# Optimization experiments

Hardware: AMD Instinct MI355X
Metric: run time of the kernel (lower is better)

## Reference

```python
import jax, jax.numpy as jnp
import numpy as np

B, T, Y, X, E, TR, R = 64, 1024, 512, 128, 512, 512, 512


def setup_inputs() -> dict:
    key = jax.random.key(0)
    ks = iter(jax.random.split(key, 48))

    def w(shape, s=0.05):
        return (jax.random.normal(next(ks), shape, jnp.float32) * s)

    z = lambda *s: jnp.zeros(s, jnp.float32)
    inp = dict(
        data=jax.random.uniform(next(ks), (B, T, Y), jnp.float32),
        eps_q=jax.random.normal(next(ks), (T, B, X), jnp.float32),
        eps_p=jax.random.normal(next(ks), (T, B, X), jnp.float32),
        # RNN (single layer, relu nonlinearity)
        rnn_Wih=w((Y, R)), rnn_Whh=w((R, R)), rnn_bih=z(R), rnn_bhh=z(R),
        h0=z(R), xq0=z(X), x0=z(X),
        # GaussianCombiner
        comb_Wxh=w((X, R)), comb_bxh=z(R),
        comb_Whm=w((R, X)), comb_bhm=z(X),
        comb_Whl=w((R, X)), comb_bhl=z(X),
        # GaussianGatedTransition
        t_Wg1=w((X, TR)), t_bg1=z(TR), t_Wg2=w((TR, X)), t_bg2=z(X),
        t_Wp1=w((X, TR)), t_bp1=z(TR), t_Wp2=w((TR, X)), t_bp2=z(X),
        t_Wmu=jnp.eye(X, dtype=jnp.float32), t_bmu=z(X),  # torch inits lin_x_to_mu to identity
        t_Wlv=w((X, X)), t_blv=z(X),
        # BernoulliEmitter
        e_W1=w((X, E)), e_b1=z(E), e_W2=w((E, E)), e_b2=z(E),
        e_W3=w((E, Y)), e_b3=z(Y),
    )
    return inp


def reference(data, eps_q, eps_p,
              rnn_Wih, rnn_Whh, rnn_bih, rnn_bhh, h0, xq0, x0,
              comb_Wxh, comb_bxh, comb_Whm, comb_bhm, comb_Whl, comb_bhl,
              t_Wg1, t_bg1, t_Wg2, t_bg2, t_Wp1, t_bp1, t_Wp2, t_bp2,
              t_Wmu, t_bmu, t_Wlv, t_blv,
              e_W1, e_b1, e_W2, e_b2, e_W3, e_b3):
    Bx = data.shape[0]

    # ---- inference RNN: run on time-reversed data, then reverse output back ----
    # precompute input projection for all steps: [T, B, R]
    x_proj = (jnp.einsum('bty,yr->btr', data[:, ::-1, :], rnn_Wih)
              + rnn_bih + rnn_bhh).transpose(1, 0, 2)

    def rnn_step(h, xp):
        h = jax.nn.relu(xp + h @ rnn_Whh)
        return h, h

    h_init = jnp.broadcast_to(h0, (Bx, R))
    _, hs = jax.lax.scan(rnn_step, h_init, x_proj)  # [T, B, R]
    rnn_out = hs[::-1]  # back to original time order, aligned with data

    # ---- inference network: sequential combiner + reparameterize ----
    def inf_step(x_prev, inputs):
        h_rnn, eps = inputs
        h_c = 0.5 * (jnp.tanh(x_prev @ comb_Wxh + comb_bxh) + h_rnn)
        mu = h_c @ comb_Whm + comb_bhm
        lv = h_c @ comb_Whl + comb_bhl
        x_t = mu + eps * jnp.exp(0.5 * lv)
        return x_t, (x_t, mu, lv)

    xq0b = jnp.broadcast_to(xq0, (Bx, X))
    _, (q_x, q_mu, q_lv) = jax.lax.scan(inf_step, xq0b, (rnn_out, eps_q))
    q_x, q_mu, q_lv = (a.transpose(1, 0, 2) for a in (q_x, q_mu, q_lv))  # [B,T,X]

    # ---- generative model: sequential gated transition ----
    def gen_step(x_prev, eps):
        gate = jax.nn.sigmoid(jax.nn.relu(x_prev @ t_Wg1 + t_bg1) @ t_Wg2 + t_bg2)
        pm = jax.nn.relu(x_prev @ t_Wp1 + t_bp1) @ t_Wp2 + t_bp2
        mu = (1.0 - gate) * (x_prev @ t_Wmu + t_bmu) + gate * pm
        lv = jax.nn.relu(pm) @ t_Wlv + t_blv
        x_t = mu + eps * jnp.exp(0.5 * lv)
        return x_t, (x_t, mu, lv)

    x0b = jnp.broadcast_to(x0, (Bx, X))
    _, (p_x, p_mu, p_lv) = jax.lax.scan(gen_step, x0b, eps_p)
    p_x, p_mu, p_lv = (a.transpose(1, 0, 2) for a in (p_x, p_mu, p_lv))  # [B,T,X]

    # ---- emitter over all (b, t) at once ----
    h1 = jax.nn.relu(jnp.einsum('btx,xe->bte', q_x, e_W1) + e_b1)
    h2 = jax.nn.relu(jnp.einsum('bte,ef->btf', h1, e_W2) + e_b2)
    y_probs = jax.nn.sigmoid(jnp.einsum('bte,ey->bty', h2, e_W3) + e_b3)

    return (q_x, q_mu, q_lv, p_x, p_mu, p_lv, y_probs)
```

## Files before the change

kernel.cpp:

```cpp
#include <hip/hip_runtime.h>
#include <stdint.h>

typedef __bf16 bf16x8 __attribute__((ext_vector_type(8)));
typedef short  s16x8  __attribute__((ext_vector_type(8)));
typedef float  f32x4  __attribute__((ext_vector_type(4)));

#define MFMA16(a, b, c) __builtin_amdgcn_mfma_f32_16x16x32_bf16((a), (b), (c), 0, 0, 0)

#define OFF_X      0ull
#define OFF_QXBF   67108864ull
#define OFF_WIH    83886080ull
#define OFF_WHH    84410368ull
#define OFF_WXH    84934656ull
#define OFF_WICAT  85065728ull
#define OFF_W1CAT  85327872ull
#define OFF_WG2    85590016ull
#define OFF_WP2    85721088ull
#define OFF_WMU    85852160ull
#define OFF_WLV    85884928ull
#define OFF_EW1    85917696ull
#define OFF_EW2    86048768ull
#define OFF_EW3    86573056ull
#define OFF_B1CAT  87097344ull
#define OFF_BICAT  87101440ull
#define OFF_HX     87102464ull
#define OFF_XPCNT  87364608ull
#define OFF_RNNF   87368704ull

#define QX_O  0ull
#define QMU_O 8388608ull
#define QLV_O 16777216ull
#define PX_O  25165824ull
#define PMU_O 33554432ull
#define PLV_O 41943040ull
#define Y_O   50331648ull

#define SMEM_SCAN 159744
#define SMEM_EMIS 133120

struct P {
  char* ws; float* out;
  const float *data, *eps_q, *eps_p;
  const float *Wih, *Whh, *bih, *bhh, *h0, *xq0, *x0;
  const float *Wxh, *bxh, *Whm, *bhm, *Whl, *bhl;
  const float *Wg1, *bg1, *Wg2, *bg2, *Wp1, *bp1, *Wp2, *bp2, *Wmu, *bmu, *Wlv, *blv;
  const float *eW1, *eb1, *eW2, *eb2, *eW3, *eb3;
};

__device__ __forceinline__ short f2bf(float f) {
  union { float f; uint32_t u; } v; v.f = f;
  uint32_t r = (v.u + 0x7FFFu + ((v.u >> 16) & 1u)) >> 16;
  return (short)(uint16_t)r;
}
__device__ __forceinline__ float bf2f(short s) {
  union { uint32_t u; float f; } v; v.u = ((uint32_t)(uint16_t)s) << 16;
  return v.f;
}
__device__ __forceinline__ bf16x8 ldfrag(const short* pp) { return *(const bf16x8*)pp; }
__device__ __forceinline__ bf16x8 cvt8p(const float* pp) {
  bf16x8 r;
#pragma unroll
  for (int i = 0; i < 8; ++i) r[i] = (__bf16)pp[i];
  return r;
}
__device__ __forceinline__ bf16x8 relu8(bf16x8 a) {
  s16x8 s = __builtin_bit_cast(s16x8, a);
#pragma unroll
  for (int i = 0; i < 8; ++i) s[i] = (s[i] < 0) ? (short)0 : s[i];
  return __builtin_bit_cast(bf16x8, s);
}

__device__ __forceinline__ void relfence() {
  asm volatile("s_waitcnt vmcnt(0)" ::: "memory");
}
__device__ __forceinline__ void st_sc16(short* pp, short v) {
  __hip_atomic_store(pp, v, __ATOMIC_RELAXED, __HIP_MEMORY_SCOPE_AGENT);
}
__device__ __forceinline__ short ld_sc16(const short* pp) {
  return __hip_atomic_load((short*)pp, __ATOMIC_RELAXED, __HIP_MEMORY_SCOPE_AGENT);
}
__device__ __forceinline__ unsigned long long ld_sc64(const void* pp) {
  return __hip_atomic_load((unsigned long long*)pp, __ATOMIC_RELAXED, __HIP_MEMORY_SCOPE_AGENT);
}
__device__ __forceinline__ bf16x8 ldfrag_sc(const short* pp) {
  union { unsigned long long q[2]; bf16x8 v; } u;
  u.q[0] = ld_sc64(pp);
  u.q[1] = ld_sc64(pp + 4);
  return u.v;
}
__device__ __forceinline__ int ldflag(int* pp) {
  return __hip_atomic_load(pp, __ATOMIC_RELAXED, __HIP_MEMORY_SCOPE_AGENT);
}
__device__ __forceinline__ void stflag(int* pp, int v) {
  __hip_atomic_store(pp, v, __ATOMIC_RELAXED, __HIP_MEMORY_SCOPE_AGENT);
}
__device__ __forceinline__ void waitf(int* f, int n, int target) {
  if (threadIdx.x < 64) {
    const int ln = threadIdx.x;
    while (1) {
      int v = (ln < n) ? ldflag(f + ln) : target;
      if (__all(v >= target)) break;
      __builtin_amdgcn_s_sleep(1);
    }
  }
  __syncthreads();
}
__device__ __forceinline__ void pubf(int* f, int val) {
  relfence();
  __syncthreads();
  if (threadIdx.x == 0) stflag(f, val);
}
__device__ __forceinline__ void cpy16(void* dst, const void* src, int n16) {
  float4* d = (float4*)dst; const float4* s = (const float4*)src;
  for (int i = threadIdx.x; i < n16; i += 256) d[i] = s[i];
}

__device__ __forceinline__ void pack_w(short* dst, const float* src, int KT, int N, int idx) {
  int tile = idx >> 9, rem = idx & 511;
  int lane = rem >> 3, j = rem & 7;
  int nt = tile / KT, kt = tile - nt * KT;
  int k = kt * 32 + ((lane >> 4) << 3) + j, n = (nt << 4) + (lane & 15);
  dst[idx] = f2bf(src[(int64_t)k * N + n]);
}

__global__ void __launch_bounds__(256) k_prep(P p) {
  char* ws = p.ws;
  const int64_t total = 1608032;
  for (int64_t i = (int64_t)blockIdx.x * 256 + threadIdx.x; i < total;
       i += (int64_t)gridDim.x * 256) {
    int64_t r = i;
    if (r < 262144) { pack_w((short*)(ws + OFF_WIH), p.Wih, 16, 512, (int)r); continue; }
    r -= 262144;
    if (r < 262144) { pack_w((short*)(ws + OFF_WHH), p.Whh, 16, 512, (int)r); continue; }
    r -= 262144;
    if (r < 65536) { pack_w((short*)(ws + OFF_WXH), p.Wxh, 4, 512, (int)r); continue; }
    r -= 65536;
    if (r < 131072) {
      int idx = (int)r;
      int tile = idx >> 9, rem = idx & 511, lane = rem >> 3, jj = rem & 7;
      int nt = tile >> 4, kt = tile & 15;
      int k = kt * 32 + ((lane >> 4) << 3) + jj, ccol = (nt << 4) + (lane & 15);
      int pair = ccol >> 7, within = ccol & 127, sub = within >> 6;
      int col = (within & 63) + (pair << 6);
      const float* s = sub ? p.Whl : p.Whm;
      ((short*)(ws + OFF_WICAT))[idx] = f2bf(s[(int64_t)k * 128 + col]);
      continue;
    }
// ... 5 lines not shown
      int k = kt * 32 + ((lane >> 4) << 3) + jj, ccol = (nt << 4) + (lane & 15);
      const float* s = (ccol < 512) ? p.Wg1 : p.Wp1;
      ((short*)(ws + OFF_W1CAT))[idx] = f2bf(s[(int64_t)k * 512 + (ccol & 511)]);
      continue;
    }
    r -= 131072;
    if (r < 65536) { pack_w((short*)(ws + OFF_WG2), p.Wg2, 16, 128, (int)r); continue; }
    r -= 65536;
    if (r < 65536) { pack_w((short*)(ws + OFF_WP2), p.Wp2, 16, 128, (int)r); continue; }
    r -= 65536;
    if (r < 16384) { pack_w((short*)(ws + OFF_WMU), p.Wmu, 4, 128, (int)r); continue; }
    r -= 16384;
    if (r < 16384) { pack_w((short*)(ws + OFF_WLV), p.Wlv, 4, 128, (int)r); continue; }
    r -= 16384;
    if (r < 65536) { pack_w((short*)(ws + OFF_EW1), p.eW1, 4, 512, (int)r); continue; }
    r -= 65536;
    if (r < 262144) { pack_w((short*)(ws + OFF_EW2), p.eW2, 16, 512, (int)r); continue; }
    r -= 262144;
    if (r < 262144) { pack_w((short*)(ws + OFF_EW3), p.eW3, 16, 512, (int)r); continue; }
    r -= 262144;
    if (r < 1024) { ((float*)(ws + OFF_B1CAT))[r] = (r < 512) ? p.bg1[r] : p.bp1[r - 512]; continue; }
    r -= 1024;
    if (r < 256) {
      int ccol = (int)r; int pair = ccol >> 7, within = ccol & 127, sub = within >> 6;
      int col = (within & 63) + (pair << 6);
      ((float*)(ws + OFF_BICAT))[ccol] = sub ? p.bhl[col] : p.bhm[col];
      continue;
    }
    r -= 256;
    ((int*)(ws + OFF_XPCNT))[r] = 0;
  }
}

__global__ void __launch_bounds__(256, 1) k_scan(P p) {
  extern __shared__ char smem[];
  char* ws = p.ws;
  const int tid = threadIdx.x;
  const int lane = tid & 63, w = tid >> 6;
  const int l16 = lane & 15, quad = lane >> 4;
  const int wg = blockIdx.x;

  short* Xb   = (short*)(ws + OFF_X);
  short* qxbf = (short*)(ws + OFF_QXBF);
  int* xp_cnt = (int*)(ws + OFF_XPCNT);

  if (wg < 64) {
    const int s = wg & 7, t0 = wg >> 3;
    const short* wih = (const short*)(ws + OFF_WIH);
    for (int tt = 0; tt < 128; ++tt) {
      const int t = t0 + (tt << 3);
      const int tsrc = 1023 - t;
      const float* arow = p.data + ((size_t)(w * 16 + l16) * 1024 + tsrc) * 512 + quad * 8;
      f32x4 acc[4] = {};
      for (int kt = 0; kt < 16; ++kt) {
        bf16x8 af = cvt8p(arow + kt * 32);
#pragma unroll
        for (int i = 0; i < 4; ++i) {
          const int nt = s * 4 + i;
          bf16x8 bw = ldfrag(wih + ((size_t)(nt * 16 + kt) * 64 + lane) * 8);
          acc[i] = MFMA16(af, bw, acc[i]);
        }
      }
      short* xrow = Xb + (size_t)t * 32768;
#pragma unroll
      for (int i = 0; i < 4; ++i) {
        const int col = (s * 4 + i) * 16 + l16;
        const float bias = p.bih[col] + p.bhh[col];
#pragma unroll
        for (int r = 0; r < 4; ++r) {
          const int row = w * 16 + quad * 4 + r;
          st_sc16(xrow + (size_t)row * 512 + col, f2bf(acc[i][r] + bias));
        }
      }
      relfence();
      __syncthreads();
      if (tid == 0) atomicAdd(xp_cnt + t, 1);
    }
    return;
  }

  if (wg < 72) {
    const int id = wg - 64, g = id >> 1, k = id & 1;
    int* rf = (int*)(ws + OFF_RNNF) + g * 4;
    short* hxb = (short*)(ws + OFF_HX);
    short* hl = (short*)smem;
    {
      const short* whh = (const short*)(ws + OFF_WHH);
      bf16x8 wb[4][16];
#pragma unroll
      for (int i = 0; i < 4; ++i) {
        const int nt = k * 16 + w * 4 + i;
#pragma unroll
        for (int kt = 0; kt < 16; ++kt)
          wb[i][kt] = ldfrag(whh + ((size_t)(nt * 16 + kt) * 64 + lane) * 8);
      }
      for (int t = 0; t < 1024; ++t) {
        if (tid < 64) {
          while (1) {
            int ok = 1;
            if (tid == 0) { if (t > 0) ok = (ldflag(rf + (1 - k)) >= t); }
            else if (tid == 1) ok = (ldflag(xp_cnt + t) >= 8);
            if (__all(ok)) break;
            __builtin_amdgcn_s_sleep(1);
          }
        }
        __syncthreads();
        bf16x8 af[16];
        short xv[4][4];
        if (t == 0) {
#pragma unroll
          for (int kt = 0; kt < 16; ++kt) af[kt] = cvt8p(p.h0 + kt * 32 + quad * 8);
        } else {
          const short* hs = hxb + (((size_t)(g * 2 + ((t - 1) & 1)) * 2 + (1 - k)) * 4096);
#pragma unroll
          for (int kt = 0; kt < 8; ++kt)
            af[(1 - k) * 8 + kt] = ldfrag_sc(hs + l16 * 256 + kt * 32 + quad * 8);
        }
        {
          const short* xrow = Xb + (size_t)t * 32768;
#pragma unroll
          for (int i = 0; i < 4; ++i) {
            const int col = k * 256 + (w * 4 + i) * 16 + l16;
#pragma unroll
            for (int r = 0; r < 4; ++r)
              xv[i][r] = ld_sc16(xrow + (size_t)(g * 16 + quad * 4 + r) * 512 + col);
          }
        }
        if (t > 0) {
#pragma unroll
          for (int kt = 0; kt < 8; ++kt)
            af[k * 8 + kt] = ldfrag(hl + l16 * 256 + kt * 32 + quad * 8);
        }
        f32x4 acc[4] = {};
#pragma unroll
        for (int kt = 0; kt < 16; ++kt)
#pragma unroll
          for (int i = 0; i < 4; ++i) acc[i] = MFMA16(af[kt], wb[i][kt], acc[i]);
        short* hdst = hxb + (((size_t)(g * 2 + (t & 1)) * 2 + k) * 4096);
        short* xrow = Xb + (size_t)t * 32768;
#pragma unroll
        for (int i = 0; i < 4; ++i) {
          const int cl = (w * 4 + i) * 16 + l16;
          const int col = k * 256 + cl;
#pragma unroll
          for (int r = 0; r < 4; ++r) {
            const int row = quad * 4 + r;
            float h = acc[i][r] + bf2f(xv[i][r]);
            const short hv = f2bf(h > 0.f ? h : 0.f);
            hl[row * 256 + cl] = hv;
            st_sc16(hdst + row * 256 + cl, hv);
            st_sc16(xrow + (size_t)(g * 16 + row) * 512 + col, hv);
          }
        }
        pubf(rf + k, t + 1);
      }
    }
    if (k == 1) return;
    waitf(rf, 2, 1024);
    const int g2 = g;
    short* ldsWxh = (short*)smem;
    short* hcl = (short*)(smem + 131072);
    short* xql = (short*)(smem + 147456);
    float* scr = (float*)(smem + 151552);
    cpy16(smem, ws + OFF_WXH, 8192);
    const short* wicat = (const short*)(ws + OFF_WICAT);
    const float* bicat = (const float*)(ws + OFF_BICAT);
    bf16x8 wbv[4][16];
    float bias2[4];
#pragma unroll
    for (int i = 0; i < 4; ++i) {
      const int nt = w * 4 + i;
#pragma unroll
      for (int kt = 0; kt < 16; ++kt)
        wbv[i][kt] = ldfrag(wicat + ((size_t)(nt * 16 + kt) * 64 + lane) * 8);
      bias2[i] = bicat[nt * 16 + l16];
    }
    float bx[8];
#pragma unroll
    for (int i = 0; i < 8; ++i) bx[i] = p.bxh[(w * 8 + i) * 16 + l16];
    __syncthreads();
    for (int t = 0; t < 1024; ++t) {
      short rv[8][4];
      {
        const short* rsrc = Xb + (size_t)(1023 - t) * 32768;
#pragma unroll
        for (int i = 0; i < 8; ++i) {
          const int ng = (w * 8 + i) * 16 + l16;
#pragma unroll
          for (int r = 0; r < 4; ++r)
            rv[i][r] = ld_sc16(rsrc + (size_t)(g2 * 16 + quad * 4 + r) * 512 + ng);
        }
      }
      float ev[8];
#pragma unroll
      for (int pp = 0; pp < 2; ++pp)
#pragma unroll
        for (int q2 = 0; q2 < 4; ++q2) {
          const int idx = tid + q2 * 256;
          const int row = idx >> 6, cl = idx & 63, col = pp * 64 + cl;
          ev[pp * 4 + q2] = p.eps_q[((size_t)t * 64 + g2 * 16 + row) * 128 + col];
        }
      bf16x8 af1[4];
      if (t == 0) {
#pragma unroll
        for (int kt = 0; kt < 4; ++kt) af1[kt] = cvt8p(p.xq0 + kt * 32 + quad * 8);
      } else {
#pragma unroll
        for (int kt = 0; kt < 4; ++kt) af1[kt] = ldfrag(xql + l16 * 128 + kt * 32 + quad * 8);
      }
      f32x4 acc1[8] = {};
#pragma unroll
      for (int kt = 0; kt < 4; ++kt)
#pragma unroll
        for (int i = 0; i < 8; ++i) {
          bf16x8 bw = ldfrag(ldsWxh + ((size_t)((w * 8 + i) * 4 + kt) * 64 + lane) * 8);
          acc1[i] = MFMA16(af1[kt], bw, acc1[i]);
        }
#pragma unroll
      for (int i = 0; i < 8; ++i) {
        const int ng = (w * 8 + i) * 16 + l16;
#pragma unroll
        for (int r = 0; r < 4; ++r) {
          const float u = acc1[i][r] + bx[i];
          const float e = __expf(2.f * u);
          const float th = 1.f - 2.f / (e + 1.f);
          const float hc = 0.5f * (th + bf2f(rv[i][r]));
          hcl[(quad * 4 + r) * 512 + ng] = f2bf(hc);
        }
      }
      __syncthreads();
      bf16x8 af2[16];
#pragma unroll
      for (int kt = 0; kt < 16; ++kt) af2[kt] = ldfrag(hcl + l16 * 512 + kt * 32 + quad * 8);
      f32x4 acc2[4] = {};
#pragma unroll
      for (int kt = 0; kt < 16; ++kt)
#pragma unroll
        for (int i = 0; i < 4; ++i) acc2[i] = MFMA16(af2[kt], wbv[i][kt], acc2[i]);
#pragma unroll
      for (int i = 0; i < 4; ++i) {
        const int catcol = (w * 4 + i) * 16 + l16;
        const int within = catcol & 127, sub = within >> 6;
        const int col = (within & 63) + ((catcol >> 7) << 6);
        float* dbase = p.out + (sub ? QLV_O : QMU_O);
#pragma unroll
        for (int r = 0; r < 4; ++r) {
          const int b = g2 * 16 + quad * 4 + r;
          dbase[(size_t)b * 131072 + (size_t)t * 128 + col] = acc2[i][r] + bias2[i];
        }
      }
#pragma unroll
      for (int pp = 0; pp < 2; ++pp) {
        if ((w >> 1) == pp) {
#pragma unroll
          for (int i = 0; i < 4; ++i) {
            const int catcol = (w * 4 + i) * 16 + l16;
            const int sub = (catcol >> 6) & 1, c6 = catcol & 63;
#pragma unroll
            for (int r = 0; r < 4; ++r)
              scr[(sub * 16 + quad * 4 + r) * 64 + c6] = acc2[i][r] + bias2[i];
          }
        }
        __syncthreads();
        {
#pragma unroll
          for (int q2 = 0; q2 < 4; ++q2) {
            const int idx = tid + q2 * 256;
            const int row = idx >> 6, cl = idx & 63, col = pp * 64 + cl;
            const int b = g2 * 16 + row;
            const float m = scr[row * 64 + cl], l = scr[(16 + row) * 64 + cl];
            const float xv = m + ev[pp * 4 + q2] * __expf(0.5f * l);
            p.out[QX_O + (size_t)b * 131072 + (size_t)t * 128 + col] = xv;
            const short xb = f2bf(xv);
            qxbf[((size_t)b * 1024 + t) * 128 + col] = xb;
            xql[row * 128 + col] = xb;
          }
        }
        __syncthreads();
      }
    }
    return;
  }

  {
    const int g3 = wg - 72;
    short* xl  = (short*)smem;
    short* u1l = (short*)(smem + 4096);
    short* pml = (short*)(smem + 36864);
    short* ldsWmu = (short*)(smem + 40960);
    short* ldsWlv = (short*)(smem + 73728);
    cpy16(smem + 40960, ws + OFF_WMU, 2048);
    cpy16(smem + 73728, ws + OFF_WLV, 2048);
    const short* w1cat = (const short*)(ws + OFF_W1CAT);
    const float* b1cat = (const float*)(ws + OFF_B1CAT);
    const short* wp2g = (const short*)(ws + OFF_WP2);
    const short* wg2g = (const short*)(ws + OFF_WG2);
    bf16x8 w1[16][4];
    float b1[16];
#pragma unroll
    for (int i = 0; i < 16; ++i) {
      const int nt = w * 16 + i;
#pragma unroll
      for (int kt = 0; kt < 4; ++kt)
        w1[i][kt] = ldfrag(w1cat + ((size_t)(nt * 4 + kt) * 64 + lane) * 8);
      b1[i] = b1cat[nt * 16 + l16];
    }
    float bp[2], bg[2], bm[2], bl[2];
#pragma unroll
    for (int i = 0; i < 2; ++i) {
      const int col = (w * 2 + i) * 16 + l16;
      bp[i] = p.bp2[col]; bg[i] = p.bg2[col]; bm[i] = p.bmu[col]; bl[i] = p.blv[col];
    }
    __syncthreads();
    for (int t = 0; t < 1024; ++t) {
      float ep[2][4];
#pragma unroll
      for (int i = 0; i < 2; ++i) {
        const int col = (w * 2 + i) * 16 + l16;
#pragma unroll
        for (int r = 0; r < 4; ++r)
          ep[i][r] = p.eps_p[((size_t)t * 64 + g3 * 16 + quad * 4 + r) * 128 + col];
      }
      bf16x8 ax[4];
      if (t == 0) {
#pragma unroll
        for (int kt = 0; kt < 4; ++kt) ax[kt] = cvt8p(p.x0 + kt * 32 + quad * 8);
      } else {
#pragma unroll
        for (int kt = 0; kt < 4; ++kt) ax[kt] = ldfrag(xl + l16 * 128 + kt * 32 + quad * 8);
      }
#pragma unroll
      for (int hf = 0; hf < 2; ++hf) {
        f32x4 a1[8] = {};
#pragma unroll
        for (int kt = 0; kt < 4; ++kt)
#pragma unroll
          for (int i = 0; i < 8; ++i) a1[i] = MFMA16(ax[kt], w1[hf * 8 + i][kt], a1[i]);
#pragma unroll
        for (int i = 0; i < 8; ++i) {
          const int c1 = (w * 16 + hf * 8 + i) * 16 + l16;
#pragma unroll
          for (int r = 0; r < 4; ++r) {
            const float u = a1[i][r] + b1[hf * 8 + i];
            u1l[(quad * 4 + r) * 1024 + c1] = f2bf(u > 0.f ? u : 0.f);
          }
        }
      }
      __syncthreads();
      f32x4 apm[2] = {}, ag[2] = {}, axm[2] = {};
#pragma unroll
      for (int ch = 0; ch < 4; ++ch) {
        bf16x8 au[4], bwp[2][4];
#pragma unroll
        for (int kt = 0; kt < 4; ++kt)
          au[kt] = ldfrag(u1l + l16 * 1024 + 512 + (ch * 4 + kt) * 32 + quad * 8);
#pragma unroll
        for (int i = 0; i < 2; ++i)
#pragma unroll
          for (int kt = 0; kt < 4; ++kt)
            bwp[i][kt] = ldfrag(wp2g + ((size_t)((w * 2 + i) * 16 + ch * 4 + kt) * 64 + lane) * 8);
#pragma unroll
        for (int kt = 0; kt < 4; ++kt)
#pragma unroll
          for (int i = 0; i < 2; ++i) apm[i] = MFMA16(au[kt], bwp[i][kt], apm[i]);
      }
#pragma unroll
      for (int ch = 0; ch < 4; ++ch) {
        bf16x8 au[4], bwg[2][4];
#pragma unroll
        for (int kt = 0; kt < 4; ++kt)
          au[kt] = ldfrag(u1l + l16 * 1024 + (ch * 4 + kt) * 32 + quad * 8);
#pragma unroll
        for (int i = 0; i < 2; ++i)
#pragma unroll
          for (int kt = 0; kt < 4; ++kt)
            bwg[i][kt] = ldfrag(wg2g + ((size_t)((w * 2 + i) * 16 + ch * 4 + kt) * 64 + lane) * 8);
#pragma unroll
        for (int kt = 0; kt < 4; ++kt)
#pragma unroll
          for (int i = 0; i < 2; ++i) ag[i] = MFMA16(au[kt], bwg[i][kt], ag[i]);
      }
#pragma unroll
      for (int kt = 0; kt < 4; ++kt)
#pragma unroll
        for (int i = 0; i < 2; ++i) {
          bf16x8 bw = ldfrag(ldsWmu + ((size_t)((w * 2 + i) * 4 + kt) * 64 + lane) * 8);
          axm[i] = MFMA16(ax[kt], bw, axm[i]);
        }
      float pmv[2][4];
#pragma unroll
      for (int i = 0; i < 2; ++i) {
        const int col = (w * 2 + i) * 16 + l16;
#pragma unroll
        for (int r = 0; r < 4; ++r) {
          pmv[i][r] = apm[i][r] + bp[i];
          pml[(quad * 4 + r) * 128 + col] = f2bf(pmv[i][r]);
        }
      }
      __syncthreads();
      bf16x8 apf[4];
#pragma unroll
      for (int kt = 0; kt < 4; ++kt)
        apf[kt] = relu8(ldfrag(pml + l16 * 128 + kt * 32 + quad * 8));
      f32x4 alv[2] = {};
#pragma unroll
      for (int kt = 0; kt < 4; ++kt)
#pragma unroll
        for (int i = 0; i < 2; ++i) {
          bf16x8 bw = ldfrag(ldsWlv + ((size_t)((w * 2 + i) * 4 + kt) * 64 + lane) * 8);
          alv[i] = MFMA16(apf[kt], bw, alv[i]);
        }
#pragma unroll
      for (int i = 0; i < 2; ++i) {
        const int col = (w * 2 + i) * 16 + l16;
#pragma unroll
        for (int r = 0; r < 4; ++r) {
          const int row = quad * 4 + r, b = g3 * 16 + row;
          const float lv = alv[i][r] + bl[i];
          const float gv = 1.f / (1.f + __expf(-(ag[i][r] + bg[i])));
          const float xmv = axm[i][r] + bm[i];
          const float mu = (1.f - gv) * xmv + gv * pmv[i][r];
          const float xv = mu + ep[i][r] * __expf(0.5f * lv);
          xl[row * 128 + col] = f2bf(xv);
          p.out[PMU_O + (size_t)b * 131072 + (size_t)t * 128 + col] = mu;
          p.out[PLV_O + (size_t)b * 131072 + (size_t)t * 128 + col] = lv;
          p.out[PX_O  + (size_t)b * 131072 + (size_t)t * 128 + col] = xv;
        }
      }
      __syncthreads();
    }
    return;
  }
}

__global__ void __launch_bounds__(256) k_emis(P p) {
  extern __shared__ char smem[];
  short* h1 = (short*)smem;
  short* h2 = (short*)(smem + 66560);
  const int tid = threadIdx.x, lane = tid & 63, w = tid >> 6;
  const int l16 = lane & 15, quad = lane >> 4;
  const size_t m0 = (size_t)blockIdx.x * 64;
  const short* qx  = (const short*)(p.ws + OFF_QXBF);
  const short* ew1 = (const short*)(p.ws + OFF_EW1);
  const short* ew2 = (const short*)(p.ws + OFF_EW2);
  const short* ew3 = (const short*)(p.ws + OFF_EW3);
  for (int nc = 0; nc < 2; ++nc) {
    f32x4 acc[4][4] = {};
    for (int kt = 0; kt < 4; ++kt) {
      bf16x8 bw[4];
#pragma unroll
      for (int i = 0; i < 4; ++i) {
        const int nt = w * 8 + nc * 4 + i;
        bw[i] = ldfrag(ew1 + ((size_t)(nt * 4 + kt) * 64 + lane) * 8);
      }
#pragma unroll
      for (int mt = 0; mt < 4; ++mt) {
        bf16x8 af = ldfrag(qx + (m0 + mt * 16 + l16) * 128 + kt * 32 + quad * 8);
#pragma unroll
        for (int i = 0; i < 4; ++i) acc[mt][i] = MFMA16(af, bw[i], acc[mt][i]);
      }
    }
#pragma unroll
// ... 74 lines not shown
}

extern "C" void kernel_launch(void* const* d_in, const int* in_sizes, int n_in,
                              void* d_out, int out_size, void* d_ws, size_t ws_size,
                              hipStream_t stream) {
  (void)in_sizes; (void)n_in; (void)out_size; (void)ws_size;
  P p;
  p.ws = (char*)d_ws; p.out = (float*)d_out;
  p.data = (const float*)d_in[0];
  p.eps_q = (const float*)d_in[1];
  p.eps_p = (const float*)d_in[2];
  p.Wih = (const float*)d_in[3]; p.Whh = (const float*)d_in[4];
  p.bih = (const float*)d_in[5]; p.bhh = (const float*)d_in[6];
  p.h0 = (const float*)d_in[7]; p.xq0 = (const float*)d_in[8]; p.x0 = (const float*)d_in[9];
  p.Wxh = (const float*)d_in[10]; p.bxh = (const float*)d_in[11];
  p.Whm = (const float*)d_in[12]; p.bhm = (const float*)d_in[13];
  p.Whl = (const float*)d_in[14]; p.bhl = (const float*)d_in[15];
  p.Wg1 = (const float*)d_in[16]; p.bg1 = (const float*)d_in[17];
  p.Wg2 = (const float*)d_in[18]; p.bg2 = (const float*)d_in[19];
  p.Wp1 = (const float*)d_in[20]; p.bp1 = (const float*)d_in[21];
  p.Wp2 = (const float*)d_in[22]; p.bp2 = (const float*)d_in[23];
  p.Wmu = (const float*)d_in[24]; p.bmu = (const float*)d_in[25];
  p.Wlv = (const float*)d_in[26]; p.blv = (const float*)d_in[27];
  p.eW1 = (const float*)d_in[28]; p.eb1 = (const float*)d_in[29];
  p.eW2 = (const float*)d_in[30]; p.eb2 = (const float*)d_in[31];
  p.eW3 = (const float*)d_in[32]; p.eb3 = (const float*)d_in[33];

  hipFuncSetAttribute(reinterpret_cast<const void*>(k_scan),
                      hipFuncAttributeMaxDynamicSharedMemorySize, SMEM_SCAN);
  hipFuncSetAttribute(reinterpret_cast<const void*>(k_emis),
                      hipFuncAttributeMaxDynamicSharedMemorySize, SMEM_EMIS);

  k_prep<<<dim3(2048), dim3(256), 0, stream>>>(p);
  k_scan<<<dim3(76), dim3(256), SMEM_SCAN, stream>>>(p);
  k_emis<<<dim3(1024), dim3(256), SMEM_EMIS, stream>>>(p);
}
```

Measured before the change: 13.88 ms.

## Run each RNN batch group in one 512-thread workgroup, dropping cross-block flag exchange

The recurrent RNN step was previously split across two workgroups per batch group, which exchanged half of the hidden state each timestep through global memory and flags. Each group now runs in a single 512-thread workgroup: Whh is held partly in registers and partly in LDS, and the hidden state is double-buffered in XOR-swizzled LDS, so each step needs only a local barrier. The combiner and transition scans are re-tiled to 8 waves with swizzled LDS and a lighter barrier, and the grid shrinks from 76 to 72 workgroups. The cost is higher register and LDS pressure per block and less parallel work on the serial RNN path.

```diff
diff --git a/kernel.cpp b/kernel.cpp
--- a/kernel.cpp
+++ b/kernel.cpp
@@ -23,9 +23,7 @@
 #define OFF_EW3    86573056ull
 #define OFF_B1CAT  87097344ull
 #define OFF_BICAT  87101440ull
-#define OFF_HX     87102464ull
 #define OFF_XPCNT  87364608ull
-#define OFF_RNNF   87368704ull
 
 #define QX_O  0ull
 #define QMU_O 8388608ull
@@ -35,7 +33,7 @@
 #define PLV_O 41943040ull
 #define Y_O   50331648ull
 
-#define SMEM_SCAN 159744
+#define SMEM_SCAN 131072
 #define SMEM_EMIS 133120
 
 struct P {
@@ -79,40 +77,14 @@
 __device__ __forceinline__ short ld_sc16(const short* pp) {
   return __hip_atomic_load((short*)pp, __ATOMIC_RELAXED, __HIP_MEMORY_SCOPE_AGENT);
 }
-__device__ __forceinline__ unsigned long long ld_sc64(const void* pp) {
-  return __hip_atomic_load((unsigned long long*)pp, __ATOMIC_RELAXED, __HIP_MEMORY_SCOPE_AGENT);
-}
-__device__ __forceinline__ bf16x8 ldfrag_sc(const short* pp) {
-  union { unsigned long long q[2]; bf16x8 v; } u;
-  u.q[0] = ld_sc64(pp);
-  u.q[1] = ld_sc64(pp + 4);
-  return u.v;
-}
 __device__ __forceinline__ int ldflag(int* pp) {
   return __hip_atomic_load(pp, __ATOMIC_RELAXED, __HIP_MEMORY_SCOPE_AGENT);
 }
-__device__ __forceinline__ void stflag(int* pp, int v) {
-  __hip_atomic_store(pp, v, __ATOMIC_RELAXED, __HIP_MEMORY_SCOPE_AGENT);
-}
-__device__ __forceinline__ void waitf(int* f, int n, int target) {
-  if (threadIdx.x < 64) {
-    const int ln = threadIdx.x;
-    while (1) {
-      int v = (ln < n) ? ldflag(f + ln) : target;
-      if (__all(v >= target)) break;
-      __builtin_amdgcn_s_sleep(1);
-    }
-  }
-  __syncthreads();
-}
-__device__ __forceinline__ void pubf(int* f, int val) {
-  relfence();
-  __syncthreads();
-  if (threadIdx.x == 0) stflag(f, val);
-}
-__device__ __forceinline__ void cpy16(void* dst, const void* src, int n16) {
-  float4* d = (float4*)dst; const float4* s = (const float4*)src;
-  for (int i = threadIdx.x; i < n16; i += 256) d[i] = s[i];
+__device__ __forceinline__ void barrier_lgkm() {
+  __builtin_amdgcn_sched_barrier(0);
+  asm volatile("s_waitcnt lgkmcnt(0)" ::: "memory");
+  __builtin_amdgcn_s_barrier();
+  __builtin_amdgcn_sched_barrier(0);
 }
 
 __device__ __forceinline__ void pack_w(short* dst, const float* src, int KT, int N, int idx) {
@@ -184,7 +156,7 @@
   }
 }
 
-__global__ void __launch_bounds__(256, 1) k_scan(P p) {
+__global__ void __launch_bounds__(512, 2) k_scan(P p) {
   extern __shared__ char smem[];
   char* ws = p.ws;
   const int tid = threadIdx.x;
@@ -198,29 +170,30 @@
 
   if (wg < 64) {
     const int s = wg & 7, t0 = wg >> 3;
+    const int mrow4 = (w & 3) * 16;
+    const int nt0 = s * 4 + (w >> 2) * 2;
     const short* wih = (const short*)(ws + OFF_WIH);
     for (int tt = 0; tt < 128; ++tt) {
       const int t = t0 + (tt << 3);
       const int tsrc = 1023 - t;
-      const float* arow = p.data + ((size_t)(w * 16 + l16) * 1024 + tsrc) * 512 + quad * 8;
-      f32x4 acc[4] = {};
+      const float* arow = p.data + ((size_t)(mrow4 + l16) * 1024 + tsrc) * 512 + quad * 8;
+      f32x4 acc[2] = {};
       for (int kt = 0; kt < 16; ++kt) {
         bf16x8 af = cvt8p(arow + kt * 32);
 #pragma unroll
-        for (int i = 0; i < 4; ++i) {
-          const int nt = s * 4 + i;
-          bf16x8 bw = ldfrag(wih + ((size_t)(nt * 16 + kt) * 64 + lane) * 8);
+        for (int i = 0; i < 2; ++i) {
+          bf16x8 bw = ldfrag(wih + ((size_t)((nt0 + i) * 16 + kt) * 64 + lane) * 8);
           acc[i] = MFMA16(af, bw, acc[i]);
         }
       }
       short* xrow = Xb + (size_t)t * 32768;
 #pragma unroll
-      for (int i = 0; i < 4; ++i) {
-        const int col = (s * 4 + i) * 16 + l16;
+      for (int i = 0; i < 2; ++i) {
+        const int col = (nt0 + i) * 16 + l16;
         const float bias = p.bih[col] + p.bhh[col];
 #pragma unroll
         for (int r = 0; r < 4; ++r) {
-          const int row = w * 16 + quad * 4 + r;
+          const int row = mrow4 + quad * 4 + r;
           st_sc16(xrow + (size_t)row * 512 + col, f2bf(acc[i][r] + bias));
         }
       }
@@ -231,355 +204,383 @@
     return;
   }
 
-  if (wg < 72) {
-    const int id = wg - 64, g = id >> 1, k = id & 1;
-    int* rf = (int*)(ws + OFF_RNNF) + g * 4;
-    short* hxb = (short*)(ws + OFF_HX);
-    short* hl = (short*)smem;
+  if (wg < 68) {
+    const int g = wg - 64;
+    short* whh_l = (short*)smem;
+    char* hbuf = smem + 98304;
     {
-      const short* whh = (const short*)(ws + OFF_WHH);
-      bf16x8 wb[4][16];
-#pragma unroll
-      for (int i = 0; i < 4; ++i) {
-        const int nt = k * 16 + w * 4 + i;
-#pragma unroll
-        for (int kt = 0; kt < 16; ++kt)
-          wb[i][kt] = ldfrag(whh + ((size_t)(nt * 16 + kt) * 64 + lane) * 8);
-      }
-      for (int t = 0; t < 1024; ++t) {
-        if (tid < 64) {
-          while (1) {
-            int ok = 1;
-            if (tid == 0) { if (t > 0) ok = (ldflag(rf + (1 - k)) >= t); }
-            else if (tid == 1) ok = (ldflag(xp_cnt + t) >= 8);
-            if (__all(ok)) break;
-            __builtin_amdgcn_s_sleep(1);
+      const float4* src4 = (const float4*)(ws + OFF_WHH);
+      float4* dst4 = (float4*)smem;
+      for (int i2 = tid; i2 < 6144; i2 += 512) {
+        const int blk = i2 >> 6, wi = i2 & 63;
+        const int nt = blk / 3, kk = blk - nt * 3;
+        dst4[(size_t)blk * 64 + wi] = src4[(size_t)(nt * 16 + 13 + kk) * 64 + wi];
+      }
+    }
+    const short* whh = (const short*)(ws + OFF_WHH);
+    bf16x8 wb[4][13];
+#pragma unroll
+    for (int i = 0; i < 4; ++i) {
+      const int nt = w * 4 + i;
+#pragma unroll
+      for (int kt = 0; kt < 13; ++kt)
+        wb[i][kt] = ldfrag(whh + ((size_t)(nt * 16 + kt) * 64 + lane) * 8);
+    }
+    __syncthreads();
+    while (ldflag(xp_cnt) < 8) __builtin_amdgcn_s_sleep(2);
+    short xv[4][4];
+#pragma unroll
+    for (int i = 0; i < 4; ++i) {
+      const int col = (w * 4 + i) * 16 + l16;
+#pragma unroll
+      for (int r = 0; r < 4; ++r)
+        xv[i][r] = ld_sc16(Xb + (size_t)(g * 16 + quad * 4 + r) * 512 + col);
+    }
+    {
+      f32x4 acc[4] = {};
+#pragma unroll
+      for (int c = 0; c < 8; ++c) {
+        bf16x8 a2[2];
+#pragma unroll
+        for (int k2 = 0; k2 < 2; ++k2) a2[k2] = cvt8p(p.h0 + (c * 2 + k2) * 32 + quad * 8);
+#pragma unroll
+        for (int k2 = 0; k2 < 2; ++k2) {
+          const int kt = c * 2 + k2;
+#pragma unroll
+          for (int i = 0; i < 4; ++i) {
+            bf16x8 bw = (kt < 13)
+                ? wb[i][kt]
+                : ldfrag(whh_l + ((size_t)((w * 4 + i) * 3 + (kt - 13)) * 64 + lane) * 8);
+            acc[i] = MFMA16(a2[k2], bw, acc[i]);
           }
         }
-        __syncthreads();
-        bf16x8 af[16];
-        short xv[4][4];
-        if (t == 0) {
-#pragma unroll
-          for (int kt = 0; kt < 16; ++kt) af[kt] = cvt8p(p.h0 + kt * 32 + quad * 8);
-        } else {
-          const short* hs = hxb + (((size_t)(g * 2 + ((t - 1) & 1)) * 2 + (1 - k)) * 4096);
-#pragma unroll
-          for (int kt = 0; kt < 8; ++kt)
-            af[(1 - k) * 8 + kt] = ldfrag_sc(hs + l16 * 256 + kt * 32 + quad * 8);
-        }
-        {
-          const short* xrow = Xb + (size_t)t * 32768;
+      }
+      char* hw = hbuf;
+      short* xrow = Xb;
+#pragma unroll
+      for (int i = 0; i < 4; ++i) {
+        const int col = (w * 4 + i) * 16 + l16;
+#pragma unroll
+        for (int r = 0; r < 4; ++r) {
+          const int row = quad * 4 + r;
+          float h = acc[i][r] + bf2f(xv[i][r]);
+          const short hv = f2bf(h > 0.f ? h : 0.f);
+          *(short*)(hw + row * 1024 + ((col * 2) ^ ((row & 7) << 4))) = hv;
+          st_sc16(xrow + (size_t)(g * 16 + row) * 512 + col, hv);
+        }
+      }
+      while (ldflag(xp_cnt + 1) < 8) __builtin_amdgcn_s_sleep(2);
+      const short* xn = Xb + 32768;
+#pragma unroll
+      for (int i = 0; i < 4; ++i) {
+        const int col = (w * 4 + i) * 16 + l16;
+#pragma unroll
+        for (int r = 0; r < 4; ++r)
+          xv[i][r] = ld_sc16(xn + (size_t)(g * 16 + quad * 4 + r) * 512 + col);
+      }
+      barrier_lgkm();
+    }
+    for (int t = 1; t < 1024; ++t) {
+      const char* hb = hbuf + ((t - 1) & 1) * 16384;
+      f32x4 acc[4] = {};
+#pragma unroll
+      for (int c = 0; c < 8; ++c) {
+        bf16x8 a2[2];
+#pragma unroll
+        for (int k2 = 0; k2 < 2; ++k2) {
+          const int kt = c * 2 + k2;
+          a2[k2] = ldfrag((const short*)(hb + l16 * 1024 +
+                     ((kt * 64 + quad * 16) ^ ((l16 & 7) << 4))));
+        }
+#pragma unroll
+        for (int k2 = 0; k2 < 2; ++k2) {
+          const int kt = c * 2 + k2;
 #pragma unroll
           for (int i = 0; i < 4; ++i) {
-            const int col = k * 256 + (w * 4 + i) * 16 + l16;
-#pragma unroll
-            for (int r = 0; r < 4; ++r)
-              xv[i][r] = ld_sc16(xrow + (size_t)(g * 16 + quad * 4 + r) * 512 + col);
+            bf16x8 bw = (kt < 13)
+                ? wb[i][kt]
+                : ldfrag(whh_l + ((size_t)((w * 4 + i) * 3 + (kt - 13)) * 64 + lane) * 8);
+            acc[i] = MFMA16(a2[k2], bw, acc[i]);
           }
         }
-        if (t > 0) {
-#pragma unroll
-          for (int kt = 0; kt < 8; ++kt)
-            af[k * 8 + kt] = ldfrag(hl + l16 * 256 + kt * 32 + quad * 8);
-        }
-        f32x4 acc[4] = {};
-#pragma unroll
-        for (int kt = 0; kt < 16; ++kt)
-#pragma unroll
-          for (int i = 0; i < 4; ++i) acc[i] = MFMA16(af[kt], wb[i][kt], acc[i]);
-        short* hdst = hxb + (((size_t)(g * 2 + (t & 1)) * 2 + k) * 4096);
-        short* xrow = Xb + (size_t)t * 32768;
+      }
+      char* hw = hbuf + (t & 1) * 16384;
+      short* xrow = Xb + (size_t)t * 32768;
+#pragma unroll
+      for (int i = 0; i < 4; ++i) {
+        const int col = (w * 4 + i) * 16 + l16;
+#pragma unroll
+        for (int r = 0; r < 4; ++r) {
+          const int row = quad * 4 + r;
+          float h = acc[i][r] + bf2f(xv[i][r]);
+          const short hv = f2bf(h > 0.f ? h : 0.f);
+          *(short*)(hw + row * 1024 + ((col * 2) ^ ((row & 7) << 4))) = hv;
+          st_sc16(xrow + (size_t)(g * 16 + row) * 512 + col, hv);
+        }
+      }
+      if (t < 1023) {
+        int* fc = xp_cnt + t + 1;
+        while (ldflag(fc) < 8) __builtin_amdgcn_s_sleep(2);
+        const short* xn = Xb + (size_t)(t + 1) * 32768;
 #pragma unroll
         for (int i = 0; i < 4; ++i) {
-          const int cl = (w * 4 + i) * 16 + l16;
-          const int col = k * 256 + cl;
-#pragma unroll
-          for (int r = 0; r < 4; ++r) {
-            const int row = quad * 4 + r;
-            float h = acc[i][r] + bf2f(xv[i][r]);
-            const short hv = f2bf(h > 0.f ? h : 0.f);
-            hl[row * 256 + cl] = hv;
-            st_sc16(hdst + row * 256 + cl, hv);
-            st_sc16(xrow + (size_t)(g * 16 + row) * 512 + col, hv);
-          }
-        }
-        pubf(rf + k, t + 1);
-      }
-    }
-    if (k == 1) return;
-    waitf(rf, 2, 1024);
+          const int col = (w * 4 + i) * 16 + l16;
+#pragma unroll
+          for (int r = 0; r < 4; ++r)
+            xv[i][r] = ld_sc16(xn + (size_t)(g * 16 + quad * 4 + r) * 512 + col);
+        }
+      }
+      barrier_lgkm();
+    }
+    relfence();
+    __syncthreads();
     const int g2 = g;
-    short* ldsWxh = (short*)smem;
-    short* hcl = (short*)(smem + 131072);
-    short* xql = (short*)(smem + 147456);
-    float* scr = (float*)(smem + 151552);
-    cpy16(smem, ws + OFF_WXH, 8192);
+    char* hcs = smem;
+    char* xqs = smem + 16384;
+    float* scr = (float*)(smem + 20480);
+    const short* wxh = (const short*)(ws + OFF_WXH);
     const short* wicat = (const short*)(ws + OFF_WICAT);
     const float* bicat = (const float*)(ws + OFF_BICAT);
-    bf16x8 wbv[4][16];
-    float bias2[4];
+    bf16x8 wa[4][4];
+    float bx[4];
 #pragma unroll
     for (int i = 0; i < 4; ++i) {
       const int nt = w * 4 + i;
+#pragma unroll
+      for (int kt = 0; kt < 4; ++kt)
+        wa[i][kt] = ldfrag(wxh + ((size_t)(nt * 4 + kt) * 64 + lane) * 8);
+      bx[i] = p.bxh[nt * 16 + l16];
+    }
+    bf16x8 wbv[2][16];
+    float bias2[2];
+#pragma unroll
+    for (int i = 0; i < 2; ++i) {
+      const int nt = w * 2 + i;
 #pragma unroll
       for (int kt = 0; kt < 16; ++kt)
         wbv[i][kt] = ldfrag(wicat + ((size_t)(nt * 16 + kt) * 64 + lane) * 8);
       bias2[i] = bicat[nt * 16 + l16];
     }
-    float bx[8];
-#pragma unroll
-    for (int i = 0; i < 8; ++i) bx[i] = p.bxh[(w * 8 + i) * 16 + l16];
-    __syncthreads();
     for (int t = 0; t < 1024; ++t) {
-      short rv[8][4];
-      {
-        const short* rsrc = Xb + (size_t)(1023 - t) * 32768;
-#pragma unroll
-        for (int i = 0; i < 8; ++i) {
-          const int ng = (w * 8 + i) * 16 + l16;
-#pragma unroll
-          for (int r = 0; r < 4; ++r)
-            rv[i][r] = ld_sc16(rsrc + (size_t)(g2 * 16 + quad * 4 + r) * 512 + ng);
-        }
-      }
-      float ev[8];
-#pragma unroll
-      for (int pp = 0; pp < 2; ++pp)
-#pragma unroll
-        for (int q2 = 0; q2 < 4; ++q2) {
-          const int idx = tid + q2 * 256;
-          const int row = idx >> 6, cl = idx & 63, col = pp * 64 + cl;
-          ev[pp * 4 + q2] = p.eps_q[((size_t)t * 64 + g2 * 16 + row) * 128 + col];
-        }
+      short rv[4][4];
+      const short* rsrc = Xb + (size_t)(1023 - t) * 32768;
+#pragma unroll
+      for (int i = 0; i < 4; ++i) {
+        const int ng = (w * 4 + i) * 16 + l16;
+#pragma unroll
+        for (int r = 0; r < 4; ++r)
+          rv[i][r] = ld_sc16(rsrc + (size_t)(g2 * 16 + quad * 4 + r) * 512 + ng);
+      }
+      float ev[4];
+#pragma unroll
+      for (int q2 = 0; q2 < 4; ++q2) {
+        const int idx = tid + q2 * 512;
+        const int row = idx >> 7, cl = idx & 127;
+        ev[q2] = p.eps_q[((size_t)t * 64 + g2 * 16 + row) * 128 + cl];
+      }
       bf16x8 af1[4];
       if (t == 0) {
 #pragma unroll
         for (int kt = 0; kt < 4; ++kt) af1[kt] = cvt8p(p.xq0 + kt * 32 + quad * 8);
       } else {
 #pragma unroll
-        for (int kt = 0; kt < 4; ++kt) af1[kt] = ldfrag(xql + l16 * 128 + kt * 32 + quad * 8);
-      }
-      f32x4 acc1[8] = {};
+        for (int kt = 0; kt < 4; ++kt)
+          af1[kt] = ldfrag((const short*)(xqs + l16 * 256 +
+                     ((kt * 64 + quad * 16) ^ ((l16 & 7) << 4))));
+      }
+      f32x4 acc1[4] = {};
 #pragma unroll
       for (int kt = 0; kt < 4; ++kt)
 #pragma unroll
-        for (int i = 0; i < 8; ++i) {
-          bf16x8 bw = ldfrag(ldsWxh + ((size_t)((w * 8 + i) * 4 + kt) * 64 + lane) * 8);
-          acc1[i] = MFMA16(af1[kt], bw, acc1[i]);
-        }
-#pragma unroll
-      for (int i = 0; i < 8; ++i) {
-        const int ng = (w * 8 + i) * 16 + l16;
+        for (int i = 0; i < 4; ++i) acc1[i] = MFMA16(af1[kt], wa[i][kt], acc1[i]);
+#pragma unroll
+      for (int i = 0; i < 4; ++i) {
+        const int ng = (w * 4 + i) * 16 + l16;
 #pragma unroll
         for (int r = 0; r < 4; ++r) {
+          const int row = quad * 4 + r;
           const float u = acc1[i][r] + bx[i];
           const float e = __expf(2.f * u);
           const float th = 1.f - 2.f / (e + 1.f);
-          const float hc = 0.5f * (th + bf2f(rv[i][r]));
-          hcl[(quad * 4 + r) * 512 + ng] = f2bf(hc);
-        }
-      }
-      __syncthreads();
-      bf16x8 af2[16];
-#pragma unroll
-      for (int kt = 0; kt < 16; ++kt) af2[kt] = ldfrag(hcl + l16 * 512 + kt * 32 + quad * 8);
-      f32x4 acc2[4] = {};
-#pragma unroll
-      for (int kt = 0; kt < 16; ++kt)
-#pragma unroll
-        for (int i = 0; i < 4; ++i) acc2[i] = MFMA16(af2[kt], wbv[i][kt], acc2[i]);
-#pragma unroll
-      for (int i = 0; i < 4; ++i) {
-        const int catcol = (w * 4 + i) * 16 + l16;
+          const float hcv = 0.5f * (th + bf2f(rv[i][r]));
+          *(short*)(hcs + row * 1024 + ((ng * 2) ^ ((row & 7) << 4))) = f2bf(hcv);
+        }
+      }
+      barrier_lgkm();
+      f32x4 acc2[2] = {};
+#pragma unroll
+      for (int c = 0; c < 4; ++c) {
+        bf16x8 a4[4];
+#pragma unroll
+        for (int k2 = 0; k2 < 4; ++k2) {
+          const int kt = c * 4 + k2;
+          a4[k2] = ldfrag((const short*)(hcs + l16 * 1024 +
+                     ((kt * 64 + quad * 16) ^ ((l16 & 7) << 4))));
+        }
+#pragma unroll
+        for (int k2 = 0; k2 < 4; ++k2)
+#pragma unroll
+          for (int i = 0; i < 2; ++i) acc2[i] = MFMA16(a4[k2], wbv[i][c * 4 + k2], acc2[i]);
+      }
+#pragma unroll
+      for (int i = 0; i < 2; ++i) {
+        const int catcol = (w * 2 + i) * 16 + l16;
         const int within = catcol & 127, sub = within >> 6;
         const int col = (within & 63) + ((catcol >> 7) << 6);
         float* dbase = p.out + (sub ? QLV_O : QMU_O);
 #pragma unroll
         for (int r = 0; r < 4; ++r) {
-          const int b = g2 * 16 + quad * 4 + r;
-          dbase[(size_t)b * 131072 + (size_t)t * 128 + col] = acc2[i][r] + bias2[i];
-        }
-      }
-#pragma unroll
-      for (int pp = 0; pp < 2; ++pp) {
-        if ((w >> 1) == pp) {
-#pragma unroll
-          for (int i = 0; i < 4; ++i) {
-            const int catcol = (w * 4 + i) * 16 + l16;
-            const int sub = (catcol >> 6) & 1, c6 = catcol & 63;
-#pragma unroll
-            for (int r = 0; r < 4; ++r)
-              scr[(sub * 16 + quad * 4 + r) * 64 + c6] = acc2[i][r] + bias2[i];
-          }
-        }
-        __syncthreads();
-        {
-#pragma unroll
-          for (int q2 = 0; q2 < 4; ++q2) {
-            const int idx = tid + q2 * 256;
-            const int row = idx >> 6, cl = idx & 63, col = pp * 64 + cl;
-            const int b = g2 * 16 + row;
-            const float m = scr[row * 64 + cl], l = scr[(16 + row) * 64 + cl];
-            const float xv = m + ev[pp * 4 + q2] * __expf(0.5f * l);
-            p.out[QX_O + (size_t)b * 131072 + (size_t)t * 128 + col] = xv;
-            const short xb = f2bf(xv);
-            qxbf[((size_t)b * 1024 + t) * 128 + col] = xb;
-            xql[row * 128 + col] = xb;
-          }
-        }
-        __syncthreads();
-      }
+          const int row = quad * 4 + r;
+          const float v = acc2[i][r] + bias2[i];
+          dbase[(size_t)(g2 * 16 + row) * 131072 + (size_t)t * 128 + col] = v;
+          scr[(sub * 16 + row) * 128 + col] = v;
+        }
+      }
+      barrier_lgkm();
+#pragma unroll
+      for (int q2 = 0; q2 < 4; ++q2) {
+        const int idx = tid + q2 * 512;
+        const int row = idx >> 7, cl = idx & 127;
+        const int b = g2 * 16 + row;
+        const float m = scr[row * 128 + cl], l = scr[(16 + row) * 128 + cl];
+        const float xvv = m + ev[q2] * __expf(0.5f * l);
+        p.out[QX_O + (size_t)b * 131072 + (size_t)t * 128 + cl] = xvv;
+        const short xb = f2bf(xvv);
+        qxbf[((size_t)b * 1024 + t) * 128 + cl] = xb;
+        *(short*)(xqs + row * 256 + ((cl * 2) ^ ((row & 7) << 4))) = xb;
+      }
+      barrier_lgkm();
     }
     return;
   }
 
   {
-    const int g3 = wg - 72;
-    short* xl  = (short*)smem;
-    short* u1l = (short*)(smem + 4096);
-    short* pml = (short*)(smem + 36864);
-    short* ldsWmu = (short*)(smem + 40960);
-    short* ldsWlv = (short*)(smem + 73728);
-    cpy16(smem + 40960, ws + OFF_WMU, 2048);
-    cpy16(smem + 73728, ws + OFF_WLV, 2048);
+    const int g3 = wg - 68;
+    short* ldsWmu = (short*)smem;
+    short* ldsWlv = (short*)(smem + 32768);
+    char* xls  = smem + 65536;
+    char* u1ls = smem + 69632;
+    char* pmls = smem + 102400;
+    {
+      const float4* s1 = (const float4*)(ws + OFF_WMU);
+      const float4* s2 = (const float4*)(ws + OFF_WLV);
+      float4* d1 = (float4*)smem;
+      float4* d2 = (float4*)(smem + 32768);
+      for (int i2 = tid; i2 < 2048; i2 += 512) { d1[i2] = s1[i2]; d2[i2] = s2[i2]; }
+    }
     const short* w1cat = (const short*)(ws + OFF_W1CAT);
     const float* b1cat = (const float*)(ws + OFF_B1CAT);
     const short* wp2g = (const short*)(ws + OFF_WP2);
     const short* wg2g = (const short*)(ws + OFF_WG2);
-    bf16x8 w1[16][4];
-    float b1[16];
-#pragma unroll
-    for (int i = 0; i < 16; ++i) {
-      const int nt = w * 16 + i;
+    bf16x8 w1[8][4];
+    float b1[8];
+#pragma unroll
+    for (int i = 0; i < 8; ++i) {
+      const int nt = w * 8 + i;
 #pragma unroll
       for (int kt = 0; kt < 4; ++kt)
         w1[i][kt] = ldfrag(w1cat + ((size_t)(nt * 4 + kt) * 64 + lane) * 8);
       b1[i] = b1cat[nt * 16 + l16];
     }
-    float bp[2], bg[2], bm[2], bl[2];
-#pragma unroll
-    for (int i = 0; i < 2; ++i) {
-      const int col = (w * 2 + i) * 16 + l16;
-      bp[i] = p.bp2[col]; bg[i] = p.bg2[col]; bm[i] = p.bmu[col]; bl[i] = p.blv[col];
-    }
+    const int colw = w * 16 + l16;
+    const float bpv = p.bp2[colw], bgv = p.bg2[colw], bmv = p.bmu[colw], blvv = p.blv[colw];
     __syncthreads();
     for (int t = 0; t < 1024; ++t) {
-      float ep[2][4];
-#pragma unroll
-      for (int i = 0; i < 2; ++i) {
-        const int col = (w * 2 + i) * 16 + l16;
-#pragma unroll
-        for (int r = 0; r < 4; ++r)
-          ep[i][r] = p.eps_p[((size_t)t * 64 + g3 * 16 + quad * 4 + r) * 128 + col];
-      }
+      float ep[4];
+#pragma unroll
+      for (int r = 0; r < 4; ++r)
+        ep[r] = p.eps_p[((size_t)t * 64 + g3 * 16 + quad * 4 + r) * 128 + colw];
       bf16x8 ax[4];
       if (t == 0) {
 #pragma unroll
         for (int kt = 0; kt < 4; ++kt) ax[kt] = cvt8p(p.x0 + kt * 32 + quad * 8);
       } else {
 #pragma unroll
-        for (int kt = 0; kt < 4; ++kt) ax[kt] = ldfrag(xl + l16 * 128 + kt * 32 + quad * 8);
+        for (int kt = 0; kt < 4; ++kt)
+          ax[kt] = ldfrag((const short*)(xls + l16 * 256 +
+                     ((kt * 64 + quad * 16) ^ ((l16 & 7) << 4))));
       }
 #pragma unroll
       for (int hf = 0; hf < 2; ++hf) {
-        f32x4 a1[8] = {};
+        f32x4 a1[4] = {};
 #pragma unroll
         for (int kt = 0; kt < 4; ++kt)
 #pragma unroll
-          for (int i = 0; i < 8; ++i) a1[i] = MFMA16(ax[kt], w1[hf * 8 + i][kt], a1[i]);
-#pragma unroll
-        for (int i = 0; i < 8; ++i) {
-          const int c1 = (w * 16 + hf * 8 + i) * 16 + l16;
+          for (int i = 0; i < 4; ++i) a1[i] = MFMA16(ax[kt], w1[hf * 4 + i][kt], a1[i]);
+#pragma unroll
+        for (int i = 0; i < 4; ++i) {
+          const int c1 = (w * 8 + hf * 4 + i) * 16 + l16;
 #pragma unroll
           for (int r = 0; r < 4; ++r) {
-            const float u = a1[i][r] + b1[hf * 8 + i];
-            u1l[(quad * 4 + r) * 1024 + c1] = f2bf(u > 0.f ? u : 0.f);
+            const int row = quad * 4 + r;
+            const float u = a1[i][r] + b1[hf * 4 + i];
+            *(short*)(u1ls + row * 2048 + ((c1 * 2) ^ ((row & 7) << 4))) = f2bf(u > 0.f ? u : 0.f);
           }
         }
       }
-      __syncthreads();
-      f32x4 apm[2] = {}, ag[2] = {}, axm[2] = {};
-#pragma unroll
-      for (int ch = 0; ch < 4; ++ch) {
-        bf16x8 au[4], bwp[2][4];
-#pragma unroll
-        for (int kt = 0; kt < 4; ++kt)
-          au[kt] = ldfrag(u1l + l16 * 1024 + 512 + (ch * 4 + kt) * 32 + quad * 8);
-#pragma unroll
-        for (int i = 0; i < 2; ++i)
-#pragma unroll
-          for (int kt = 0; kt < 4; ++kt)
-            bwp[i][kt] = ldfrag(wp2g + ((size_t)((w * 2 + i) * 16 + ch * 4 + kt) * 64 + lane) * 8);
-#pragma unroll
-        for (int kt = 0; kt < 4; ++kt)
-#pragma unroll
-          for (int i = 0; i < 2; ++i) apm[i] = MFMA16(au[kt], bwp[i][kt], apm[i]);
-      }
-#pragma unroll
-      for (int ch = 0; ch < 4; ++ch) {
-        bf16x8 au[4], bwg[2][4];
-#pragma unroll
-        for (int kt = 0; kt < 4; ++kt)
-          au[kt] = ldfrag(u1l + l16 * 1024 + (ch * 4 + kt) * 32 + quad * 8);
-#pragma unroll
-        for (int i = 0; i < 2; ++i)
-#pragma unroll
-          for (int kt = 0; kt < 4; ++kt)
-            bwg[i][kt] = ldfrag(wg2g + ((size_t)((w * 2 + i) * 16 + ch * 4 + kt) * 64 + lane) * 8);
-#pragma unroll
-        for (int kt = 0; kt < 4; ++kt)
-#pragma unroll
-          for (int i = 0; i < 2; ++i) ag[i] = MFMA16(au[kt], bwg[i][kt], ag[i]);
-      }
+      barrier_lgkm();
+      f32x4 apm = {}, ag = {}, axm = {};
+#pragma unroll
+      for (int c = 0; c < 8; ++c) {
+        bf16x8 bpf[2], bgf[2];
+#pragma unroll
+        for (int k2 = 0; k2 < 2; ++k2) {
+          bpf[k2] = ldfrag(wp2g + ((size_t)(w * 16 + c * 2 + k2) * 64 + lane) * 8);
+          bgf[k2] = ldfrag(wg2g + ((size_t)(w * 16 + c * 2 + k2) * 64 + lane) * 8);
+        }
+        bf16x8 aup[2], aug[2];
+#pragma unroll
+        for (int k2 = 0; k2 < 2; ++k2) {
+          const int kt = c * 2 + k2;
+          aup[k2] = ldfrag((const short*)(u1ls + l16 * 2048 +
+                      ((1024 + kt * 64 + quad * 16) ^ ((l16 & 7) << 4))));
+          aug[k2] = ldfrag((const short*)(u1ls + l16 * 2048 +
+                      ((kt * 64 + quad * 16) ^ ((l16 & 7) << 4))));
+        }
+#pragma unroll
+        for (int k2 = 0; k2 < 2; ++k2) {
+          apm = MFMA16(aup[k2], bpf[k2], apm);
+          ag  = MFMA16(aug[k2], bgf[k2], ag);
+        }
+      }
+#pragma unroll
+      for (int kt = 0; kt < 4; ++kt) {
+        bf16x8 bw = ldfrag(ldsWmu + ((size_t)(w * 4 + kt) * 64 + lane) * 8);
+        axm = MFMA16(ax[kt], bw, axm);
+      }
+      float pmv[4];
+#pragma unroll
+      for (int r = 0; r < 4; ++r) {
+        const int row = quad * 4 + r;
+        pmv[r] = apm[r] + bpv;
+        *(short*)(pmls + row * 256 + ((colw * 2) ^ ((row & 7) << 4))) = f2bf(pmv[r]);
+      }
+      barrier_lgkm();
+      bf16x8 apf[4];
 #pragma unroll
       for (int kt = 0; kt < 4; ++kt)
-#pragma unroll
-        for (int i = 0; i < 2; ++i) {
-          bf16x8 bw = ldfrag(ldsWmu + ((size_t)((w * 2 + i) * 4 + kt) * 64 + lane) * 8);
-          axm[i] = MFMA16(ax[kt], bw, axm[i]);
-        }
-      float pmv[2][4];
-#pragma unroll
-      for (int i = 0; i < 2; ++i) {
-        const int col = (w * 2 + i) * 16 + l16;
-#pragma unroll
-        for (int r = 0; r < 4; ++r) {
-          pmv[i][r] = apm[i][r] + bp[i];
-          pml[(quad * 4 + r) * 128 + col] = f2bf(pmv[i][r]);
-        }
-      }
-      __syncthreads();
-      bf16x8 apf[4];
-#pragma unroll
-      for (int kt = 0; kt < 4; ++kt)
-        apf[kt] = relu8(ldfrag(pml + l16 * 128 + kt * 32 + quad * 8));
-      f32x4 alv[2] = {};
-#pragma unroll
-      for (int kt = 0; kt < 4; ++kt)
-#pragma unroll
-        for (int i = 0; i < 2; ++i) {
-          bf16x8 bw = ldfrag(ldsWlv + ((size_t)((w * 2 + i) * 4 + kt) * 64 + lane) * 8);
-          alv[i] = MFMA16(apf[kt], bw, alv[i]);
-        }
-#pragma unroll
-      for (int i = 0; i < 2; ++i) {
-        const int col = (w * 2 + i) * 16 + l16;
-#pragma unroll
-        for (int r = 0; r < 4; ++r) {
-          const int row = quad * 4 + r, b = g3 * 16 + row;
-          const float lv = alv[i][r] + bl[i];
-          const float gv = 1.f / (1.f + __expf(-(ag[i][r] + bg[i])));
-          const float xmv = axm[i][r] + bm[i];
-          const float mu = (1.f - gv) * xmv + gv * pmv[i][r];
-          const float xv = mu + ep[i][r] * __expf(0.5f * lv);
-          xl[row * 128 + col] = f2bf(xv);
-          p.out[PMU_O + (size_t)b * 131072 + (size_t)t * 128 + col] = mu;
-          p.out[PLV_O + (size_t)b * 131072 + (size_t)t * 128 + col] = lv;
-          p.out[PX_O  + (size_t)b * 131072 + (size_t)t * 128 + col] = xv;
-        }
-      }
-      __syncthreads();
+        apf[kt] = relu8(ldfrag((const short*)(pmls + l16 * 256 +
+                    ((kt * 64 + quad * 16) ^ ((l16 & 7) << 4)))));
+      f32x4 alv = {};
+#pragma unroll
+      for (int kt = 0; kt < 4; ++kt) {
+        bf16x8 bw = ldfrag(ldsWlv + ((size_t)(w * 4 + kt) * 64 + lane) * 8);
+        alv = MFMA16(apf[kt], bw, alv);
+      }
+#pragma unroll
+      for (int r = 0; r < 4; ++r) {
+        const int row = quad * 4 + r, b = g3 * 16 + row;
+        const float lv = alv[r] + blvv;
+        const float gv = 1.f / (1.f + __expf(-(ag[r] + bgv)));
+        const float xmv = axm[r] + bmv;
+        const float mu = (1.f - gv) * xmv + gv * pmv[r];
+        const float xvv = mu + ep[r] * __expf(0.5f * lv);
+        *(short*)(xls + row * 256 + ((colw * 2) ^ ((row & 7) << 4))) = f2bf(xvv);
+        p.out[PMU_O + (size_t)b * 131072 + (size_t)t * 128 + colw] = mu;
+        p.out[PLV_O + (size_t)b * 131072 + (size_t)t * 128 + colw] = lv;
+        p.out[PX_O  + (size_t)b * 131072 + (size_t)t * 128 + colw] = xvv;
+      }
+      barrier_lgkm();
     }
     return;
   }
@@ -720,6 +721,6 @@
                       hipFuncAttributeMaxDynamicSharedMemorySize, SMEM_EMIS);
 
   k_prep<<<dim3(2048), dim3(256), 0, stream>>>(p);
-  k_scan<<<dim3(76), dim3(256), SMEM_SCAN, stream>>>(p);
+  k_scan<<<dim3(72), dim3(512), SMEM_SCAN, stream>>>(p);
   k_emis<<<dim3(1024), dim3(256), SMEM_EMIS, stream>>>(p);
 }
```

Measured after the change: 12.99 ms. 1.07x faster.
